# Performance work log

Hardware: AMD Instinct MI355X
Metric: run time of the kernel (lower is better)

The kernel has to match this reference:

```python
import jax, jax.numpy as jnp
import numpy as np

EPS = 1e-5

@jax.custom_vjp
def binarize(x):
    # sign with sign(0)->+1, as in typical BNN implementations
    return jnp.where(x >= 0, 1.0, -1.0).astype(x.dtype)

def _bin_fwd(x):
    return binarize(x), x

def _bin_bwd(x, g):
    # hardtanh straight-through estimator
    return (g * (jnp.abs(x) <= 1.0).astype(g.dtype),)

binarize.defvjp(_bin_fwd, _bin_bwd)

def bconv3x3(x, w, stride=1):
    bx = binarize(x)
    bw = binarize(w)
    return jax.lax.conv_general_dilated(
        bx, bw, window_strides=(stride, stride), padding=[(1, 1), (1, 1)],
        dimension_numbers=("NCHW", "OIHW", "NCHW"))

def bn(x, gamma, beta, mean, var):
    inv = gamma / jnp.sqrt(var + EPS)
    return x * inv[None, :, None, None] + (beta - mean * inv)[None, :, None, None]

def channel_shuffle(x, groups=2):
    b, c, h, w = x.shape
    x = x.reshape(b, groups, c // groups, h, w)
    x = jnp.transpose(x, (0, 2, 1, 3, 4))
    return x.reshape(b, c, h, w)

def hardtanh(x):
    return jnp.clip(x, -1.0, 1.0)

def setup_inputs() -> dict:
    key = jax.random.key(0)
    ks = jax.random.split(key, 13)
    P = 128
    inp = {
        "x": jax.random.normal(ks[0], (32, 2 * P, 56, 56), jnp.float32),
        "w1": jax.random.normal(ks[1], (P, P, 3, 3), jnp.float32) * 0.05,
        "w2": jax.random.normal(ks[2], (P, P, 3, 3), jnp.float32) * 0.05,
        "bn1_gamma": jax.random.uniform(ks[3], (P,), jnp.float32, 0.5, 1.5),
        "bn1_beta": jax.random.normal(ks[4], (P,), jnp.float32) * 0.1,
        "bn1_mean": jax.random.normal(ks[5], (P,), jnp.float32),
        "bn1_var": jax.random.uniform(ks[6], (P,), jnp.float32, 0.5, 1.5),
        "bn2_gamma": jax.random.uniform(ks[7], (P,), jnp.float32, 0.5, 1.5),
        "bn2_beta": jax.random.normal(ks[8], (P,), jnp.float32) * 0.1,
        "bn2_mean": jax.random.normal(ks[9], (P,), jnp.float32),
        "bn2_var": jax.random.uniform(ks[10], (P,), jnp.float32, 0.5, 1.5),
        "move0_bias": jax.random.normal(ks[11], (P,), jnp.float32) * 0.01,
        "move1_bias": jax.random.normal(ks[12], (P,), jnp.float32) * 0.01,
    }
    return inp

def reference(x, w1, w2, bn1_gamma, bn1_beta, bn1_mean, bn1_var,
              bn2_gamma, bn2_beta, bn2_mean, bn2_var, move0_bias, move1_bias):
    P = w1.shape[0]
    # split into active / idle halves
    x_act, x_idle = x[:, :P], x[:, P:]
    residual = x_act
    out = bn(bconv3x3(x_act, w1, stride=1), bn1_gamma, bn1_beta, bn1_mean, bn1_var)
    out = hardtanh(out + residual)
    x_idle = x_idle + move0_bias[None, :, None, None]
    out = channel_shuffle(jnp.concatenate([out, x_idle], axis=1))
    x_act2, x_idle2 = out[:, :P], out[:, P:]
    residual = x_act2
    out = bn(bconv3x3(x_act2, w2, stride=1), bn2_gamma, bn2_beta, bn2_mean, bn2_var)
    out = hardtanh(out + residual)
    x_idle2 = x_idle2 + move1_bias[None, :, None, None]
    out = channel_shuffle(jnp.concatenate([out, x_idle2], axis=1))
    return out
```

## Files before the change

kernel.cpp:

```cpp
#include <hip/hip_runtime.h>
#include <stdint.h>


#define HH 56
#define WW 56
#define HW 3136
#define NBATCH 32
#define NPX (NBATCH * HW)

#define WS_W1B   0u
#define WS_W2B   18432u
#define WS_BN    36864u
#define WS_BITS2 40960u
#define WS_BITS1 1646592u
#define WS_RES1  3252224u

#define PC(a,b) (__popc((a).x ^ (b).x) + __popc((a).y ^ (b).y) + \
                 __popc((a).z ^ (b).z) + __popc((a).w ^ (b).w))

__global__ __launch_bounds__(256) void prep_kernel(
    const float* __restrict__ w1, const float* __restrict__ w2,
    const float* __restrict__ g1, const float* __restrict__ b1,
    const float* __restrict__ m1, const float* __restrict__ v1,
    const float* __restrict__ g2, const float* __restrict__ b2,
    const float* __restrict__ m2, const float* __restrict__ v2,
    uint4* __restrict__ w1b, uint4* __restrict__ w2b, float* __restrict__ bnc)
{
    int t = blockIdx.x * 256 + threadIdx.x;
    if (t < 2304) {
        const float* w = (t < 1152) ? w1 : w2;
        uint4* dst = (t < 1152) ? w1b : w2b;
        int tt = (t < 1152) ? t : t - 1152;
        int o = tt / 9, tap = tt % 9;
        const float* wp = w + (size_t)o * 1152 + tap;
        uint32_t b[4];
        #pragma unroll
        for (int wd = 0; wd < 4; ++wd) {
            uint32_t acc = 0;
            #pragma unroll
            for (int bi = 0; bi < 32; ++bi) {
                float wv = wp[(size_t)(wd * 32 + bi) * 9];
                acc |= (wv >= 0.0f ? 1u : 0u) << bi;
            }
            b[wd] = acc;
        }
        dst[o * 9 + tap] = make_uint4(b[0], b[1], b[2], b[3]);
    } else if (t < 2432) {
        int c = t - 2304;
        float i1 = __fdiv_rn(g1[c], __fsqrt_rn(__fadd_rn(v1[c], 1e-5f)));
        bnc[c]       = i1;
        bnc[128 + c] = __fsub_rn(b1[c], __fmul_rn(m1[c], i1));
        float i2 = __fdiv_rn(g2[c], __fsqrt_rn(__fadd_rn(v2[c], 1e-5f)));
        bnc[256 + c] = i2;
        bnc[384 + c] = __fsub_rn(b2[c], __fmul_rn(m2[c], i2));
    }
}

__global__ __launch_bounds__(256) void binpack_kernel(
    const float* __restrict__ x, const float* __restrict__ move0,
    const float* __restrict__ move1,
    uint4* __restrict__ bits1, uint4* __restrict__ bits2,
    float* __restrict__ out)
{
    const int g = blockIdx.x / 392;
    const int px = (blockIdx.x % 392) * 256 + threadIdx.x;
    const int n = px / HW, poff = px % HW;
    const float* xn = x + (size_t)n * 256 * HW + poff;

    if (g < 2) {
        const int cb = g * 64;
        uint32_t w0 = 0, w1 = 0;
        #pragma unroll
        for (int c = 0; c < 32; ++c)
            w0 |= (xn[(size_t)(cb + c) * HW] >= 0.0f ? 1u : 0u) << c;
        #pragma unroll
        for (int c = 0; c < 32; ++c)
            w1 |= (xn[(size_t)(cb + 32 + c) * HW] >= 0.0f ? 1u : 0u) << c;
        ((uint2*)&bits1[px])[g] = make_uint2(w0, w1);
    } else if (g == 2) {
        uint32_t w0 = 0, w1 = 0, w2 = 0, w3 = 0;
        #pragma unroll
        for (int k = 0; k < 64; ++k) {
            float s = __fadd_rn(xn[(size_t)(128 + k) * HW], move0[k]);
            uint32_t m = (s >= 0.0f ? 1u : 0u) << (2 * (k & 15) + 1);
            if ((k >> 4) == 0) w0 |= m; else if ((k >> 4) == 1) w1 |= m;
            else if ((k >> 4) == 2) w2 |= m; else w3 |= m;
        }
        bits2[px] = make_uint4(w0, w1, w2, w3);
    } else {
        const int mb = (g - 3) * 32;
        for (int mm = 0; mm < 32; ++mm) {
            int m = mb + mm;
            float v = __fadd_rn(__fadd_rn(xn[(size_t)(192 + m) * HW],
                                          move0[64 + m]), move1[2 * m + 1]);
            out[(size_t)(n * 256 + 4 * m + 3) * HW + poff] = v;
        }
    }
}


__global__ __launch_bounds__(448) void conv1_kernel(
    const float* __restrict__ x, const uint4* __restrict__ w1b,
    const float* __restrict__ bnc, const float* __restrict__ move1,
    const uint4* __restrict__ bits1, uint4* __restrict__ bits2,
    uint2* __restrict__ res1, float* __restrict__ out)
{
    const int b = blockIdx.x;
    const int js = b & 7;
    const int s = b >> 3;
    const int n = s / 7, si = s % 7;
    const int tid = threadIdx.x;

    __shared__ uint4 sb[562];
    __shared__ uint4 wl[144];

    const int poff = 448 * si + tid;
    const float* xn = x + (size_t)n * 256 * HW;
    const size_t pxi = (size_t)n * HW + poff;

    float rres[16];
    #pragma unroll
    for (int jj = 0; jj < 16; ++jj)
        rres[jj] = xn[(size_t)(js * 16 + jj) * HW + poff];
    uint32_t oldrmw = 0;
    if (js < 4) oldrmw = ((const uint32_t*)(bits2 + pxi))[js];

    const uint4* bsrc = bits1 + (size_t)n * HW;
    const int base = 448 * si - 57;
    for (int i = tid; i < 562; i += 448) {
        int g = base + i;
        g = (g < 0) ? 0 : ((g > HW - 1) ? HW - 1 : g);
        sb[i] = bsrc[g];
    }
    for (int i = tid; i < 144; i += 448) wl[i] = w1b[js * 144 + i];
    __syncthreads();

    const int row = poff / WW, col = poff % WW;
    const int rok0 = (row >= 1), rok2 = (row <= HH - 2);
    const int cok0 = (col >= 1), cok2 = (col <= WW - 2);
    const uint32_t rs0 = rok0 ? ~0u : 0u, rs2 = rok2 ? ~0u : 0u;
    const uint32_t csL = cok0 ? ~0u : 0u, csR = cok2 ? ~0u : 0u;
    const int nvbase = ((1 + rok0 + rok2) * (1 + cok0 + cok2)) << 7;
    const uint4 i00 = sb[tid];       const uint4 i01 = sb[tid + 1];
    const uint4 i02 = sb[tid + 2];   const uint4 i10 = sb[tid + 56];
    const uint4 i11 = sb[tid + 57];  const uint4 i12 = sb[tid + 58];
    const uint4 i20 = sb[tid + 112]; const uint4 i21 = sb[tid + 113];
    const uint4 i22 = sb[tid + 114];

    uint32_t bw = 0;
    uint32_t q0 = 0, q1 = 0, q2 = 0, q3 = 0;

    #pragma unroll
    for (int jj = 0; jj < 16; ++jj) {
        const int j = js * 16 + jj;
        const uint4* wt = &wl[jj * 9];
        int acc = 0;
        acc += PC(wt[0], i00) & (int)(rs0 & csL);
        acc += PC(wt[1], i01) & (int)rs0;
        acc += PC(wt[2], i02) & (int)(rs0 & csR);
        acc += PC(wt[3], i10) & (int)csL;
        acc += PC(wt[4], i11);
        acc += PC(wt[5], i12) & (int)csR;
        acc += PC(wt[6], i20) & (int)(rs2 & csL);
        acc += PC(wt[7], i21) & (int)rs2;
        acc += PC(wt[8], i22) & (int)(rs2 & csR);
        float convf = (float)(nvbase - (acc << 1));
        float bno = __fadd_rn(__fmul_rn(convf, bnc[j]), bnc[128 + j]);
        float v2 = __fadd_rn(bno, rres[jj]);
        float vc = fminf(fmaxf(v2, -1.0f), 1.0f);
        if (js < 4) {
            bw |= (v2 >= 0.0f ? 1u : 0u) << (2 * jj);
            uint32_t q = (uint32_t)(uint8_t)(int8_t)__float2int_rn(
                __fmul_rn(vc, 127.0f));
            uint32_t sh = 8 * (jj & 3);
            if (jj < 4)       q0 |= q << sh;
            else if (jj < 8)  q1 |= q << sh;
            else if (jj < 12) q2 |= q << sh;
            else              q3 |= q << sh;
        } else {
            int m = j - 64;
            out[(size_t)(n * 256 + 4 * m + 1) * HW + poff] =
                __fadd_rn(vc, move1[2 * m]);
        }
    }
    if (js < 4) {
        res1[(size_t)(2 * js) * NPX + pxi]     = make_uint2(q0, q1);
        res1[(size_t)(2 * js + 1) * NPX + pxi] = make_uint2(q2, q3);
        uint32_t* dst = (uint32_t*)(bits2 + pxi);
        dst[js] = oldrmw | bw;
    }
}

__global__ __launch_bounds__(448) void conv2_kernel(
    const float* __restrict__ x, const uint4* __restrict__ w2b,
    const float* __restrict__ bnc, const float* __restrict__ move0,
    const uint4* __restrict__ bits2, const uint2* __restrict__ res1,
    float* __restrict__ out)
{
    const int b = blockIdx.x;
    const int js = b & 7;
    const int s = b >> 3;
    const int n = s / 7, si = s % 7;
    const int tid = threadIdx.x;

    __shared__ uint4 sb[562];
    __shared__ uint4 wl[144];

    const int poff = 448 * si + tid;
    const float* xn = x + (size_t)n * 256 * HW;
    const size_t pxi = (size_t)n * HW + poff;

    const uint2 rq = res1[(size_t)js * NPX + pxi];
    float ro[8];
    #pragma unroll
    for (int k = 0; k < 8; ++k)
        ro[k] = xn[(size_t)(128 + js * 8 + k) * HW + poff];

    const uint4* bsrc = bits2 + (size_t)n * HW;
    const int base = 448 * si - 57;
    for (int i = tid; i < 562; i += 448) {
        int g = base + i;
        g = (g < 0) ? 0 : ((g > HW - 1) ? HW - 1 : g);
        sb[i] = bsrc[g];
    }
    for (int i = tid; i < 144; i += 448) wl[i] = w2b[js * 144 + i];
    __syncthreads();

    const int row = poff / WW, col = poff % WW;
    const int rok0 = (row >= 1), rok2 = (row <= HH - 2);
    const int cok0 = (col >= 1), cok2 = (col <= WW - 2);
    const uint32_t rs0 = rok0 ? ~0u : 0u, rs2 = rok2 ? ~0u : 0u;
    const uint32_t csL = cok0 ? ~0u : 0u, csR = cok2 ? ~0u : 0u;
    const int nvbase = ((1 + rok0 + rok2) * (1 + cok0 + cok2)) << 7;
    const uint4 i00 = sb[tid];       const uint4 i01 = sb[tid + 1];
    const uint4 i02 = sb[tid + 2];   const uint4 i10 = sb[tid + 56];
    const uint4 i11 = sb[tid + 57];  const uint4 i12 = sb[tid + 58];
    const uint4 i20 = sb[tid + 112]; const uint4 i21 = sb[tid + 113];
    const uint4 i22 = sb[tid + 114];

    #pragma unroll
    for (int jj = 0; jj < 16; ++jj) {
        const int j = js * 16 + jj;
        const uint4* wt = &wl[jj * 9];
        int acc = 0;
        acc += PC(wt[0], i00) & (int)(rs0 & csL);
        acc += PC(wt[1], i01) & (int)rs0;
        acc += PC(wt[2], i02) & (int)(rs0 & csR);
        acc += PC(wt[3], i10) & (int)csL;
        acc += PC(wt[4], i11);
        acc += PC(wt[5], i12) & (int)csR;
        acc += PC(wt[6], i20) & (int)(rs2 & csL);
        acc += PC(wt[7], i21) & (int)rs2;
        acc += PC(wt[8], i22) & (int)(rs2 & csR);
        float convf = (float)(nvbase - (acc << 1));
        float bno = __fadd_rn(__fmul_rn(convf, bnc[256 + j]), bnc[384 + j]);
        float resv;
        if (j & 1) {
            resv = __fadd_rn(ro[jj >> 1], move0[j >> 1]);
        } else {
            int bidx = jj >> 1;
            uint32_t wq = (bidx < 4) ? rq.x : rq.y;
            int8_t q = (int8_t)(uint8_t)(wq >> (8 * (bidx & 3)));
            resv = __fmul_rn(__int2float_rn((int)q), 1.0f / 127.0f);
        }
        float v2 = __fadd_rn(bno, resv);
        float vc = fminf(fmaxf(v2, -1.0f), 1.0f);
        out[(size_t)(n * 256 + 2 * j) * HW + poff] = vc;
    }
}

extern "C" void kernel_launch(void* const* d_in, const int* in_sizes, int n_in,
                              void* d_out, int out_size, void* d_ws, size_t ws_size,
                              hipStream_t stream)
{
    const float* x   = (const float*)d_in[0];
    const float* w1  = (const float*)d_in[1];
    const float* w2  = (const float*)d_in[2];
    const float* g1  = (const float*)d_in[3];
    const float* b1  = (const float*)d_in[4];
    const float* m1  = (const float*)d_in[5];
    const float* v1  = (const float*)d_in[6];
    const float* g2  = (const float*)d_in[7];
    const float* b2  = (const float*)d_in[8];
    const float* m2  = (const float*)d_in[9];
    const float* v2  = (const float*)d_in[10];
    const float* mv0 = (const float*)d_in[11];
    const float* mv1 = (const float*)d_in[12];

    uint8_t* ws = (uint8_t*)d_ws;
    uint4* w1b = (uint4*)(ws + WS_W1B);
    uint4* w2b = (uint4*)(ws + WS_W2B);
    float* bnc = (float*)(ws + WS_BN);
    uint4* bits2 = (uint4*)(ws + WS_BITS2);
    uint4* bits1 = (uint4*)(ws + WS_BITS1);
    uint2* res1 = (uint2*)(ws + WS_RES1);
    float* outp = (float*)d_out;

    hipLaunchKernelGGL(prep_kernel, dim3(10), dim3(256), 0, stream,
                       w1, w2, g1, b1, m1, v1, g2, b2, m2, v2, w1b, w2b, bnc);
    hipLaunchKernelGGL(binpack_kernel, dim3(392 * 5), dim3(256), 0, stream,
                       x, mv0, mv1, bits1, bits2, outp);
    hipLaunchKernelGGL(conv1_kernel, dim3(224 * 8), dim3(448), 0, stream,
                       x, w1b, bnc, mv1, bits1, bits2, res1, outp);
    hipLaunchKernelGGL(conv2_kernel, dim3(224 * 8), dim3(448), 0, stream,
                       x, w2b, bnc, mv0, bits2, res1, outp);
}
```

Measured before the change: 121.5 us.

## Fold prep into binpack launch and split conv1 output channels across more blocks

Merges the weight-binarisation and BN-constant prep kernel into the binpack kernel as ten extra blocks, removing one launch. Conv1 now has each block compute 8 output channels instead of 16, doubling the grid to 3584 blocks and halving per-thread register arrays and the shared-memory weight tile. The bits2 update becomes a 16-bit store per block, which removes the 32-bit read-modify-write shared between blocks. The cost is that each block reloads the 562-entry bit halo tile, so twice as many blocks repeat that load.

```diff
diff --git a/kernel.cpp b/kernel.cpp
--- a/kernel.cpp
+++ b/kernel.cpp
@@ -18,50 +18,50 @@
 #define PC(a,b) (__popc((a).x ^ (b).x) + __popc((a).y ^ (b).y) + \
                  __popc((a).z ^ (b).z) + __popc((a).w ^ (b).w))
 
-__global__ __launch_bounds__(256) void prep_kernel(
+__global__ __launch_bounds__(256) void binpack_kernel(
+    const float* __restrict__ x, const float* __restrict__ move0,
+    const float* __restrict__ move1,
     const float* __restrict__ w1, const float* __restrict__ w2,
     const float* __restrict__ g1, const float* __restrict__ b1,
     const float* __restrict__ m1, const float* __restrict__ v1,
     const float* __restrict__ g2, const float* __restrict__ b2,
     const float* __restrict__ m2, const float* __restrict__ v2,
-    uint4* __restrict__ w1b, uint4* __restrict__ w2b, float* __restrict__ bnc)
-{
-    int t = blockIdx.x * 256 + threadIdx.x;
-    if (t < 2304) {
-        const float* w = (t < 1152) ? w1 : w2;
-        uint4* dst = (t < 1152) ? w1b : w2b;
-        int tt = (t < 1152) ? t : t - 1152;
-        int o = tt / 9, tap = tt % 9;
-        const float* wp = w + (size_t)o * 1152 + tap;
-        uint32_t b[4];
-        #pragma unroll
-        for (int wd = 0; wd < 4; ++wd) {
-            uint32_t acc = 0;
-            #pragma unroll
-            for (int bi = 0; bi < 32; ++bi) {
-                float wv = wp[(size_t)(wd * 32 + bi) * 9];
-                acc |= (wv >= 0.0f ? 1u : 0u) << bi;
-            }
-            b[wd] = acc;
-        }
-        dst[o * 9 + tap] = make_uint4(b[0], b[1], b[2], b[3]);
-    } else if (t < 2432) {
-        int c = t - 2304;
-        float i1 = __fdiv_rn(g1[c], __fsqrt_rn(__fadd_rn(v1[c], 1e-5f)));
-        bnc[c]       = i1;
-        bnc[128 + c] = __fsub_rn(b1[c], __fmul_rn(m1[c], i1));
-        float i2 = __fdiv_rn(g2[c], __fsqrt_rn(__fadd_rn(v2[c], 1e-5f)));
-        bnc[256 + c] = i2;
-        bnc[384 + c] = __fsub_rn(b2[c], __fmul_rn(m2[c], i2));
-    }
-}
-
-__global__ __launch_bounds__(256) void binpack_kernel(
-    const float* __restrict__ x, const float* __restrict__ move0,
-    const float* __restrict__ move1,
     uint4* __restrict__ bits1, uint4* __restrict__ bits2,
+    uint4* __restrict__ w1b, uint4* __restrict__ w2b, float* __restrict__ bnc,
     float* __restrict__ out)
 {
+    if (blockIdx.x >= 1960) {
+        int t = (blockIdx.x - 1960) * 256 + threadIdx.x;
+        if (t < 2304) {
+            const float* w = (t < 1152) ? w1 : w2;
+            uint4* dst = (t < 1152) ? w1b : w2b;
+            int tt = (t < 1152) ? t : t - 1152;
+            int o = tt / 9, tap = tt % 9;
+            const float* wp = w + (size_t)o * 1152 + tap;
+            uint32_t b[4];
+            #pragma unroll
+            for (int wd = 0; wd < 4; ++wd) {
+                uint32_t acc = 0;
+                #pragma unroll
+                for (int bi = 0; bi < 32; ++bi) {
+                    float wv = wp[(size_t)(wd * 32 + bi) * 9];
+                    acc |= (wv >= 0.0f ? 1u : 0u) << bi;
+                }
+                b[wd] = acc;
+            }
+            dst[o * 9 + tap] = make_uint4(b[0], b[1], b[2], b[3]);
+        } else if (t < 2432) {
+            int c = t - 2304;
+            float i1 = __fdiv_rn(g1[c], __fsqrt_rn(__fadd_rn(v1[c], 1e-5f)));
+            bnc[c]       = i1;
+            bnc[128 + c] = __fsub_rn(b1[c], __fmul_rn(m1[c], i1));
+            float i2 = __fdiv_rn(g2[c], __fsqrt_rn(__fadd_rn(v2[c], 1e-5f)));
+            bnc[256 + c] = i2;
+            bnc[384 + c] = __fsub_rn(b2[c], __fmul_rn(m2[c], i2));
+        }
+        return;
+    }
+
     const int g = blockIdx.x / 392;
     const int px = (blockIdx.x % 392) * 256 + threadIdx.x;
     const int n = px / HW, poff = px % HW;
@@ -69,24 +69,24 @@
 
     if (g < 2) {
         const int cb = g * 64;
-        uint32_t w0 = 0, w1 = 0;
+        uint32_t w0 = 0, w1v = 0;
         #pragma unroll
         for (int c = 0; c < 32; ++c)
             w0 |= (xn[(size_t)(cb + c) * HW] >= 0.0f ? 1u : 0u) << c;
         #pragma unroll
         for (int c = 0; c < 32; ++c)
-            w1 |= (xn[(size_t)(cb + 32 + c) * HW] >= 0.0f ? 1u : 0u) << c;
-        ((uint2*)&bits1[px])[g] = make_uint2(w0, w1);
+            w1v |= (xn[(size_t)(cb + 32 + c) * HW] >= 0.0f ? 1u : 0u) << c;
+        ((uint2*)&bits1[px])[g] = make_uint2(w0, w1v);
     } else if (g == 2) {
-        uint32_t w0 = 0, w1 = 0, w2 = 0, w3 = 0;
+        uint32_t w0 = 0, w1v = 0, w2v = 0, w3 = 0;
         #pragma unroll
         for (int k = 0; k < 64; ++k) {
             float s = __fadd_rn(xn[(size_t)(128 + k) * HW], move0[k]);
             uint32_t m = (s >= 0.0f ? 1u : 0u) << (2 * (k & 15) + 1);
-            if ((k >> 4) == 0) w0 |= m; else if ((k >> 4) == 1) w1 |= m;
-            else if ((k >> 4) == 2) w2 |= m; else w3 |= m;
-        }
-        bits2[px] = make_uint4(w0, w1, w2, w3);
+            if ((k >> 4) == 0) w0 |= m; else if ((k >> 4) == 1) w1v |= m;
+            else if ((k >> 4) == 2) w2v |= m; else w3 |= m;
+        }
+        bits2[px] = make_uint4(w0, w1v, w2v, w3);
     } else {
         const int mb = (g - 3) * 32;
         for (int mm = 0; mm < 32; ++mm) {
@@ -106,24 +106,24 @@
     uint2* __restrict__ res1, float* __restrict__ out)
 {
     const int b = blockIdx.x;
-    const int js = b & 7;
-    const int s = b >> 3;
+    const int js = b & 15;
+    const int s = b >> 4;
     const int n = s / 7, si = s % 7;
     const int tid = threadIdx.x;
 
     __shared__ uint4 sb[562];
-    __shared__ uint4 wl[144];
+    __shared__ uint4 wl[72];
 
     const int poff = 448 * si + tid;
     const float* xn = x + (size_t)n * 256 * HW;
     const size_t pxi = (size_t)n * HW + poff;
 
-    float rres[16];
+    float rres[8];
     #pragma unroll
-    for (int jj = 0; jj < 16; ++jj)
-        rres[jj] = xn[(size_t)(js * 16 + jj) * HW + poff];
-    uint32_t oldrmw = 0;
-    if (js < 4) oldrmw = ((const uint32_t*)(bits2 + pxi))[js];
+    for (int jj = 0; jj < 8; ++jj)
+        rres[jj] = xn[(size_t)(js * 8 + jj) * HW + poff];
+    uint32_t old16 = 0;
+    if (js < 8) old16 = ((const uint16_t*)(bits2 + pxi))[js];
 
     const uint4* bsrc = bits1 + (size_t)n * HW;
     const int base = 448 * si - 57;
@@ -132,7 +132,7 @@
         g = (g < 0) ? 0 : ((g > HW - 1) ? HW - 1 : g);
         sb[i] = bsrc[g];
     }
-    for (int i = tid; i < 144; i += 448) wl[i] = w1b[js * 144 + i];
+    if (tid < 72) wl[tid] = w1b[js * 72 + tid];
     __syncthreads();
 
     const int row = poff / WW, col = poff % WW;
@@ -147,12 +147,12 @@
     const uint4 i20 = sb[tid + 112]; const uint4 i21 = sb[tid + 113];
     const uint4 i22 = sb[tid + 114];
 
-    uint32_t bw = 0;
-    uint32_t q0 = 0, q1 = 0, q2 = 0, q3 = 0;
+    uint32_t bw = old16;
+    uint32_t q0 = 0, q1 = 0;
 
     #pragma unroll
-    for (int jj = 0; jj < 16; ++jj) {
-        const int j = js * 16 + jj;
+    for (int jj = 0; jj < 8; ++jj) {
+        const int j = js * 8 + jj;
         const uint4* wt = &wl[jj * 9];
         int acc = 0;
         acc += PC(wt[0], i00) & (int)(rs0 & csL);
@@ -168,26 +168,21 @@
         float bno = __fadd_rn(__fmul_rn(convf, bnc[j]), bnc[128 + j]);
         float v2 = __fadd_rn(bno, rres[jj]);
         float vc = fminf(fmaxf(v2, -1.0f), 1.0f);
-        if (js < 4) {
+        if (js < 8) {
             bw |= (v2 >= 0.0f ? 1u : 0u) << (2 * jj);
             uint32_t q = (uint32_t)(uint8_t)(int8_t)__float2int_rn(
                 __fmul_rn(vc, 127.0f));
             uint32_t sh = 8 * (jj & 3);
-            if (jj < 4)       q0 |= q << sh;
-            else if (jj < 8)  q1 |= q << sh;
-            else if (jj < 12) q2 |= q << sh;
-            else              q3 |= q << sh;
+            if (jj < 4) q0 |= q << sh; else q1 |= q << sh;
         } else {
             int m = j - 64;
             out[(size_t)(n * 256 + 4 * m + 1) * HW + poff] =
                 __fadd_rn(vc, move1[2 * m]);
         }
     }
-    if (js < 4) {
-        res1[(size_t)(2 * js) * NPX + pxi]     = make_uint2(q0, q1);
-        res1[(size_t)(2 * js + 1) * NPX + pxi] = make_uint2(q2, q3);
-        uint32_t* dst = (uint32_t*)(bits2 + pxi);
-        dst[js] = oldrmw | bw;
+    if (js < 8) {
+        res1[(size_t)js * NPX + pxi] = make_uint2(q0, q1);
+        ((uint16_t*)(bits2 + pxi))[js] = (uint16_t)bw;
     }
 }
 
@@ -296,11 +291,10 @@
     uint2* res1 = (uint2*)(ws + WS_RES1);
     float* outp = (float*)d_out;
 
-    hipLaunchKernelGGL(prep_kernel, dim3(10), dim3(256), 0, stream,
-                       w1, w2, g1, b1, m1, v1, g2, b2, m2, v2, w1b, w2b, bnc);
-    hipLaunchKernelGGL(binpack_kernel, dim3(392 * 5), dim3(256), 0, stream,
-                       x, mv0, mv1, bits1, bits2, outp);
-    hipLaunchKernelGGL(conv1_kernel, dim3(224 * 8), dim3(448), 0, stream,
+    hipLaunchKernelGGL(binpack_kernel, dim3(392 * 5 + 10), dim3(256), 0, stream,
+                       x, mv0, mv1, w1, w2, g1, b1, m1, v1, g2, b2, m2, v2,
+                       bits1, bits2, w1b, w2b, bnc, outp);
+    hipLaunchKernelGGL(conv1_kernel, dim3(224 * 16), dim3(448), 0, stream,
                        x, w1b, bnc, mv1, bits1, bits2, res1, outp);
     hipLaunchKernelGGL(conv2_kernel, dim3(224 * 8), dim3(448), 0, stream,
                        x, w2b, bnc, mv0, bits2, res1, outp);
```

New measurement: 115.0 us. -5.4%, faster.
